# Kernel tuning notes

Hardware: AMD Instinct MI355X
Metric: run time of the kernel (lower is better)

## Reference

```python
import jax, jax.numpy as jnp
import numpy as np

# Standard NF4 quantization codebook (bitsandbytes values)
_NF4_CB = np.array([
    -1.0, -0.6961928009986877, -0.5250730514526367, -0.39491748809814453,
    -0.28444138169288635, -0.18477343022823334, -0.09105003625154495, 0.0,
    0.07958029955625534, 0.16093020141124725, 0.24611230194568634, 0.33791524171829224,
    0.44070982933044434, 0.5626170039176941, 0.7229568362236023, 1.0], dtype=np.float32)

B, L, H, E, DFF = 2, 2048, 2048, 8, 8192
BLK = 512  # NF4 quantization block size (b_idx = h // 512 in kernel)


def setup_inputs() -> dict:
    key = jax.random.key(0)
    ks = jax.random.split(key, 8)
    N = B * L
    x = jax.random.normal(ks[0], (B, L, H), dtype=jnp.float32)
    router_w = jax.random.normal(ks[1], (H, E), dtype=jnp.float32) * 0.02
    # packed NF4: one byte = two 4-bit codebook indices (low nibble -> even h)
    nf4 = jax.random.randint(ks[2], (N, E, H // 2), 0, 256, dtype=jnp.int32)
    mean = jax.random.normal(ks[3], (N, E, H // BLK), dtype=jnp.float32) * 0.01
    std = jax.random.uniform(ks[4], (N, E, H // BLK), dtype=jnp.float32) + 0.5
    codebook = jnp.asarray(_NF4_CB)
    w1 = jax.random.normal(ks[5], (H, DFF), dtype=jnp.float32) * 0.02
    w2 = jax.random.normal(ks[6], (DFF, H), dtype=jnp.float32) * 0.02
    return {"x": x, "router_w": router_w, "nf4": nf4, "mean": mean,
            "std": std, "codebook": codebook, "w1": w1, "w2": w2}


def reference(x, router_w, nf4, mean, std, codebook, w1, w2):
    b, l, h = x.shape
    n = b * l
    e = router_w.shape[1]
    xf = x.reshape(n, h)

    # shared expert MLP (base_mlp): Linear -> GELU -> Linear
    mlp = jax.nn.gelu(xf @ w1) @ w2  # [N, H]

    # router: logits in fp32, softmax, cast to fp16 as the kernel does
    logits = xf @ router_w  # [N, E]
    probs = jax.nn.softmax(logits, axis=-1).astype(jnp.float16).astype(jnp.float32)

    # NF4 unpack: low nibble -> even h, high nibble -> odd h
    low = nf4 & 15
    high = (nf4 >> 4) & 15
    idx = jnp.stack([low, high], axis=-1).reshape(n, e, h)  # interleave -> [N,E,H]
    vals = codebook[idx]  # codebook gather, [N,E,H]

    # per-block (512) rescale: val*std + mean
    nb = mean.shape[-1]
    blk = h // nb
    dq = (vals.reshape(n, e, nb, blk) * std[..., None] + mean[..., None]).reshape(n, e, h)

    # weighted expert mix + MLP residual add
    moe = jnp.einsum('ne,neh->nh', probs, dq)
    return (moe + mlp).reshape(b, l, h)
```

## Files before the change

### kernel.cpp

```cpp
#include <hip/hip_runtime.h>
#include <hip/hip_bf16.h>
#include <hip/hip_fp16.h>

#define H 2048
#define E 8
#define DFF 8192
#define NTOK 4096
#define NB 4

typedef _Float16 f16x8 __attribute__((ext_vector_type(8)));
typedef float f32x4 __attribute__((ext_vector_type(4)));

#define AS1 __attribute__((address_space(1)))
#define AS3 __attribute__((address_space(3)))

__device__ __forceinline__ void gl_lds16(const void* g, void* l) {
    __builtin_amdgcn_global_load_lds((const AS1 unsigned int*)g,
                                     (AS3 unsigned int*)l, 16, 0, 0);
}

__device__ __forceinline__ float gelu_f(float x) {
    float u = 0.7978845608028654f * x * (1.0f + 0.044715f * x * x);
    float t = fabsf(u);
    float e = __expf(-2.0f * t);
    float th = (1.0f - e) / (1.0f + e);
    th = copysignf(th, u);
    return 0.5f * x * (1.0f + th);
}

__global__ __launch_bounds__(256) void router_cast_kernel(
    const float* __restrict__ x, const float* __restrict__ rw,
    float* __restrict__ probs, _Float16* __restrict__ xh)
{
    int n = blockIdx.x, t = threadIdx.x;
    float acc[E];
#pragma unroll
    for (int e = 0; e < E; ++e) acc[e] = 0.f;
    const float* xr = x + (size_t)n * H;
#pragma unroll
    for (int k = 0; k < H / 256; ++k) {
        int h = t + k * 256;
        float xv = xr[h];
        xh[(size_t)n * H + h] = (_Float16)xv;
        const float4* r4 = reinterpret_cast<const float4*>(rw + (size_t)h * E);
        float4 a = r4[0], b = r4[1];
        acc[0] += xv * a.x; acc[1] += xv * a.y; acc[2] += xv * a.z; acc[3] += xv * a.w;
        acc[4] += xv * b.x; acc[5] += xv * b.y; acc[6] += xv * b.z; acc[7] += xv * b.w;
    }
#pragma unroll
    for (int e = 0; e < E; ++e) {
        float v = acc[e];
#pragma unroll
        for (int o = 32; o > 0; o >>= 1) v += __shfl_down(v, o, 64);
        acc[e] = v;
    }
    __shared__ float red[4][E];
    int wave = t >> 6, lane = t & 63;
    if (lane == 0) {
#pragma unroll
        for (int e = 0; e < E; ++e) red[wave][e] = acc[e];
    }
    __syncthreads();
    if (t == 0) {
        float lg[E];
        float mx = -1e30f;
#pragma unroll
        for (int e = 0; e < E; ++e) {
            lg[e] = red[0][e] + red[1][e] + red[2][e] + red[3][e];
            mx = fmaxf(mx, lg[e]);
        }
        float s = 0.f;
#pragma unroll
        for (int e = 0; e < E; ++e) { lg[e] = expf(lg[e] - mx); s += lg[e]; }
        float inv = 1.f / s;
#pragma unroll
        for (int e = 0; e < E; ++e) {
            float p = lg[e] * inv;
            p = __half2float(__float2half(p));
            probs[(size_t)n * E + e] = p;
        }
    }
}

__global__ __launch_bounds__(256) void transpose_cast_kernel(
    const float* __restrict__ src, _Float16* __restrict__ dst, int R, int C)
{
    __shared__ float tile[32][33];
    int tx = threadIdx.x & 31, ty = threadIdx.x >> 5;
    int c0 = blockIdx.x * 32, r0 = blockIdx.y * 32;
#pragma unroll
    for (int i = ty; i < 32; i += 8)
        tile[i][tx] = src[(size_t)(r0 + i) * C + c0 + tx];
    __syncthreads();
#pragma unroll
    for (int i = ty; i < 32; i += 8)
        dst[(size_t)(c0 + i) * R + r0 + tx] = (_Float16)tile[tx][i];
}

__global__ __launch_bounds__(256) void moe_kernel(
    const int* __restrict__ nf4, const float* __restrict__ mean,
    const float* __restrict__ stdv, const float* __restrict__ cb,
    const float* __restrict__ probs, float* __restrict__ moe)
{
    int n = blockIdx.x, t = threadIdx.x;
    __shared__ float cbl[32];
    __shared__ float ps[E][NB];
    __shared__ float cmean[NB];
    if (t < 16) { float v = cb[t]; cbl[t] = v; cbl[t + 16] = v; }
    else if (t >= 32 && t < 64) {
        int e = (t - 32) >> 2, b = t & 3;
        ps[e][b] = probs[(size_t)n * E + e] * stdv[((size_t)n * E + e) * NB + b];
    } else if (t >= 64 && t < 68) {
        int b = t - 64; float s = 0.f;
        for (int e = 0; e < E; ++e)
            s += probs[(size_t)n * E + e] * mean[((size_t)n * E + e) * NB + b];
        cmean[b] = s;
    }
    __syncthreads();
    int cboff = (t & 1) << 4;
    const int* w = nf4 + (size_t)n * (E * H / 2);
    float2* outp = reinterpret_cast<float2*>(moe + (size_t)n * H);
#pragma unroll
    for (int k = 0; k < 4; ++k) {
        int j = t + k * 256;
        float psr[E];
#pragma unroll
        for (int e = 0; e < E; ++e) psr[e] = ps[e][k];
        float cm = cmean[k];
        float aL = cm, aH = cm;
#pragma unroll
        for (int e = 0; e < E; ++e) {
            int word = w[e * (H / 2) + j];
            aL += psr[e] * cbl[(word & 15) + cboff];
            aH += psr[e] * cbl[((word >> 4) & 15) + cboff];
        }
        outp[j] = make_float2(aL, aH);
    }
}

template <int EPI, int MAP>
__global__ __launch_bounds__(512, 2) void gemm8p_kernel(
    const _Float16* __restrict__ A, const _Float16* __restrict__ Bt,
    const float* __restrict__ addsrc, void* __restrict__ outv,
    float* __restrict__ aux, int K, int LDK, int N)
{
    __shared__ uint4 lds_u4[131072 / 16];
    char* lds = (char*)lds_u4;
    char* R0 = lds;
    char* R1 = lds + 65536;

    int t = threadIdx.x;
    int id = blockIdx.x;
    int xcd = id & 7, chunk = id >> 3;
    int by, bx, ks = 0;
    if constexpr (MAP == 0) {
        by = (xcd & 1) * 8 + (chunk & 7);
        bx = (xcd >> 1) * 8 + (chunk >> 3);
    } else {
        by = (xcd >> 1) * 4 + (chunk & 3);
        bx = (xcd & 1) * 4 + ((chunk >> 2) & 3);
        ks = chunk >> 4;
    }
    int m0 = by * 256, n0 = bx * 256;
    int koff = ks * K;

    const unsigned short* sA = (const unsigned short*)A
        + (size_t)(m0 + (t & 255)) * LDK + koff + (t >> 8) * 8;
    const unsigned short* sB = (const unsigned short*)Bt
        + (size_t)(n0 + (t & 255)) * LDK + koff + (t >> 8) * 8;
    unsigned dstT = (unsigned)t * 16;

    int lane = t & 63, wave = t >> 6;
    int wr = wave >> 2, wc = wave & 3;
    int mb = wr * 128, nb = wc * 64;
    int q = lane >> 4, m16 = lane & 15;

    unsigned aBase = (unsigned)(mb + m16) * 16u;
    unsigned bBase = 32768u + (unsigned)(nb + m16) * 16u;

    f32x4 acc[8][4] = {};
    f16x8 af[8], bL[4], bH[4];

#define STG_A(Wb, T, s) do { \
    gl_lds16(sA + (size_t)(T) * 64 + (s) * 16,      (Wb) + (s) * 8192 + dstT); \
    gl_lds16(sA + (size_t)(T) * 64 + (s) * 16 + 16, (Wb) + (s) * 8192 + 8192 + dstT); } while (0)
#define STG_B(Wb, T, s) do { \
    gl_lds16(sB + (size_t)(T) * 64 + (s) * 16,      (Wb) + 32768 + (s) * 8192 + dstT); \
    gl_lds16(sB + (size_t)(T) * 64 + (s) * 16 + 16, (Wb) + 32768 + (s) * 8192 + 8192 + dstT); } while (0)
#define RD_A(Rb, ih) do { \
    _Pragma("unroll") for (int il = 0; il < 4; ++il) \
    _Pragma("unroll") for (int kh = 0; kh < 2; ++kh) \
        af[il * 2 + kh] = *(const f16x8*)((Rb) + aBase + \
            (unsigned)(kh * 16384 + q * 4096 + (ih) * 1024 + il * 256)); } while (0)
#define RD_B(Rb, jh, dst) do { \
    _Pragma("unroll") for (int jl = 0; jl < 2; ++jl) \
    _Pragma("unroll") for (int kh = 0; kh < 2; ++kh) \
        dst[jl * 2 + kh] = *(const f16x8*)((Rb) + bBase + \
            (unsigned)(kh * 16384 + q * 4096 + (jh) * 512 + jl * 256)); } while (0)
#define MMQ(ih, bfr, j0) do { \
    __builtin_amdgcn_s_setprio(1); \
    _Pragma("unroll") for (int il = 0; il < 4; ++il) \
    _Pragma("unroll") for (int jl = 0; jl < 2; ++jl) \
    _Pragma("unroll") for (int kh = 0; kh < 2; ++kh) \
        acc[(ih) * 4 + il][(j0) + jl] = __builtin_amdgcn_mfma_f32_16x16x32_f16( \
            af[il * 2 + kh], bfr[jl * 2 + kh], acc[(ih) * 4 + il][(j0) + jl], 0, 0, 0); \
    __builtin_amdgcn_s_setprio(0); } while (0)
#define BARR  asm volatile("s_barrier" ::: "memory")
#define LGKM0 asm volatile("s_waitcnt lgkmcnt(0)" ::: "memory")

    STG_A(R0, 0, 0); STG_A(R0, 0, 2);
    STG_B(R0, 0, 0); STG_B(R0, 0, 2);
    STG_A(R1, 1, 0);
    asm volatile("s_waitcnt vmcnt(2)" ::: "memory");
    BARR;

    int NIT = K / 128;
    for (int i = 0; i < NIT; ++i) {
        int T0 = 2 * i, T1 = 2 * i + 1;
        bool more = (i + 1 < NIT);

        STG_A(R1, T1, 2);
        RD_A(R0, 0); RD_B(R0, 0, bL);
        BARR; LGKM0;
        MMQ(0, bL, 0);
        BARR;
        STG_B(R1, T1, 0);
        RD_B(R0, 1, bH);
        BARR; LGKM0;
        MMQ(0, bH, 2);
        BARR;
        STG_B(R1, T1, 2);
        RD_A(R0, 1);
        BARR; LGKM0;
        MMQ(1, bH, 2);
        BARR;
        if (more) STG_A(R0, T0 + 2, 0);
        MMQ(1, bL, 0);
        if (more) asm volatile("s_waitcnt vmcnt(2)" ::: "memory");
        else      asm volatile("s_waitcnt vmcnt(0)" ::: "memory");
        BARR;

        if (more) STG_A(R0, T0 + 2, 2);
        RD_A(R1, 0); RD_B(R1, 0, bL);
        BARR; LGKM0;
        MMQ(0, bL, 0);
        BARR;
        if (more) STG_B(R0, T0 + 2, 0);
        RD_B(R1, 1, bH);
        BARR; LGKM0;
        MMQ(0, bH, 2);
        BARR;
        if (more) STG_B(R0, T0 + 2, 2);
        RD_A(R1, 1);
        BARR; LGKM0;
        MMQ(1, bH, 2);
        BARR;
        if (more) STG_A(R1, T1 + 2, 0);
        MMQ(1, bL, 0);
        if (more) asm volatile("s_waitcnt vmcnt(2)" ::: "memory");
        else      asm volatile("s_waitcnt vmcnt(0)" ::: "memory");
        BARR;
    }

#pragma unroll
    for (int i = 0; i < 8; ++i)
#pragma unroll
        for (int j = 0; j < 4; ++j) {
            int row = m0 + mb + i * 16 + q * 4;
            int col = n0 + nb + j * 16 + m16;
#pragma unroll
            for (int rix = 0; rix < 4; ++rix) {
                float v = acc[i][j][rix];
                size_t o = (size_t)(row + rix) * N + col;
                if constexpr (EPI == 0) {
                    ((_Float16*)outv)[o] = (_Float16)gelu_f(v);
                } else {
                    if (ks == 0) ((float*)outv)[o] = v + addsrc[o];
                    else         aux[o] = v;
                }
            }
        }
#undef STG_A
#undef STG_B
#undef RD_A
#undef RD_B
#undef MMQ
#undef BARR
#undef LGKM0
}

__global__ __launch_bounds__(256) void combine_kernel(
    float* __restrict__ out, const float* __restrict__ part)
{
    size_t base = (size_t)blockIdx.x * 256 + threadIdx.x;
    const float4* p4 = (const float4*)part;
    float4* o4 = (float4*)out;
#pragma unroll
    for (int s = 0; s < 4; ++s) {
        size_t i = base + (size_t)s * 524288;
        float4 a = o4[i], b = p4[i];
        o4[i] = make_float4(a.x + b.x, a.y + b.y, a.z + b.z, a.w + b.w);
    }
}

extern "C" void kernel_launch(void* const* d_in, const int* in_sizes, int n_in,
                              void* d_out, int out_size, void* d_ws, size_t ws_size,
                              hipStream_t stream) {
    const float* x    = (const float*)d_in[0];
    const float* rw   = (const float*)d_in[1];
    const int*   nf4  = (const int*)d_in[2];
    const float* mean = (const float*)d_in[3];
    const float* stdv = (const float*)d_in[4];
    const float* cb   = (const float*)d_in[5];
    const float* w1   = (const float*)d_in[6];
    const float* w2   = (const float*)d_in[7];
    float* out = (float*)d_out;

    char* ws = (char*)d_ws;
    float* probs      = (float*)ws;
    float* moe        = (float*)(ws + 131072);
    _Float16* xh      = (_Float16*)(ws + 33685504);
    _Float16* w1t     = (_Float16*)(ws + 50462720);
    _Float16* w2t     = (_Float16*)(ws + 84017152);
    _Float16* hid     = (_Float16*)(ws + 117571584);
    float* pbuf       = (float*)(ws + 50462720);

    router_cast_kernel<<<NTOK, 256, 0, stream>>>(x, rw, probs, xh);
    transpose_cast_kernel<<<dim3(DFF / 32, H / 32), 256, 0, stream>>>(w1, w1t, H, DFF);
    transpose_cast_kernel<<<dim3(H / 32, DFF / 32), 256, 0, stream>>>(w2, w2t, DFF, H);
    moe_kernel<<<NTOK, 256, 0, stream>>>(nf4, mean, stdv, cb, probs, moe);
    gemm8p_kernel<0, 0><<<512, 512, 0, stream>>>(xh, w1t, nullptr, (void*)hid,
                                                 nullptr, H, H, DFF);
    gemm8p_kernel<1, 1><<<256, 512, 0, stream>>>(hid, w2t, moe, (void*)out,
                                                 pbuf, DFF / 2, DFF, H);
    combine_kernel<<<2048, 256, 0, stream>>>(out, pbuf);
}
```

Measured before the change: 790.6 us.

## Fuse router and NF4 MoE kernels, vectorize moe loads and widen transpose tiles

Merges the router/softmax kernel with the NF4 dequant-mix kernel so probabilities stay in shared memory instead of going through a global buffer, saving one launch. The MoE part now reads int4 vectors and writes two float4s per thread rather than strided scalar ints. The weight transpose-cast moves from 32x32 to 64x64 tiles with float4 loads and packed half2 stores. The fused kernel adds an extra barrier and does the NF4 work on the same block as the router reduction.

New measurement: 737.0 us. 6.8% less time.

```diff
diff --git a/kernel.cpp b/kernel.cpp
--- a/kernel.cpp
+++ b/kernel.cpp
@@ -9,6 +9,7 @@
 #define NB 4
 
 typedef _Float16 f16x8 __attribute__((ext_vector_type(8)));
+typedef _Float16 f16x2 __attribute__((ext_vector_type(2)));
 typedef float f32x4 __attribute__((ext_vector_type(4)));
 
 #define AS1 __attribute__((address_space(1)))
@@ -28,11 +29,19 @@
     return 0.5f * x * (1.0f + th);
 }
 
-__global__ __launch_bounds__(256) void router_cast_kernel(
+__global__ __launch_bounds__(256) void router_moe_kernel(
     const float* __restrict__ x, const float* __restrict__ rw,
-    float* __restrict__ probs, _Float16* __restrict__ xh)
+    const int* __restrict__ nf4, const float* __restrict__ mean,
+    const float* __restrict__ stdv, const float* __restrict__ cb,
+    _Float16* __restrict__ xh, float* __restrict__ moe)
 {
     int n = blockIdx.x, t = threadIdx.x;
+    __shared__ float red[4][E];
+    __shared__ float pr[E];
+    __shared__ float cbl[32];
+    __shared__ float ps[E][NB];
+    __shared__ float cmean[NB];
+
     float acc[E];
 #pragma unroll
     for (int e = 0; e < E; ++e) acc[e] = 0.f;
@@ -54,7 +63,6 @@
         for (int o = 32; o > 0; o >>= 1) v += __shfl_down(v, o, 64);
         acc[e] = v;
     }
-    __shared__ float red[4][E];
     int wave = t >> 6, lane = t & 63;
     if (lane == 0) {
 #pragma unroll
@@ -76,65 +84,72 @@
 #pragma unroll
         for (int e = 0; e < E; ++e) {
             float p = lg[e] * inv;
-            p = __half2float(__float2half(p));
-            probs[(size_t)n * E + e] = p;
+            pr[e] = __half2float(__float2half(p));
         }
     }
+    __syncthreads();
+
+    if (t < 16) { float v = cb[t]; cbl[t] = v; cbl[t + 16] = v; }
+    else if (t >= 32 && t < 64) {
+        int e = (t - 32) >> 2, b = t & 3;
+        ps[e][b] = pr[e] * stdv[((size_t)n * E + e) * NB + b];
+    } else if (t >= 64 && t < 68) {
+        int b = t - 64; float s = 0.f;
+        for (int e = 0; e < E; ++e)
+            s += pr[e] * mean[((size_t)n * E + e) * NB + b];
+        cmean[b] = s;
+    }
+    __syncthreads();
+
+    int b = t >> 6;
+    int cboff = (t & 1) << 4;
+    const int4* w4 = reinterpret_cast<const int4*>(nf4 + (size_t)n * (E * H / 2));
+    float o[8];
+    float cm = cmean[b];
+#pragma unroll
+    for (int u = 0; u < 8; ++u) o[u] = cm;
+#pragma unroll
+    for (int e = 0; e < E; ++e) {
+        int4 wv = w4[e * 256 + t];
+        float pse = ps[e][b];
+        int w0 = wv.x, w1 = wv.y, w2 = wv.z, w3 = wv.w;
+        o[0] += pse * cbl[(w0 & 15) + cboff];
+        o[1] += pse * cbl[((w0 >> 4) & 15) + cboff];
+        o[2] += pse * cbl[(w1 & 15) + cboff];
+        o[3] += pse * cbl[((w1 >> 4) & 15) + cboff];
+        o[4] += pse * cbl[(w2 & 15) + cboff];
+        o[5] += pse * cbl[((w2 >> 4) & 15) + cboff];
+        o[6] += pse * cbl[(w3 & 15) + cboff];
+        o[7] += pse * cbl[((w3 >> 4) & 15) + cboff];
+    }
+    float4* op = reinterpret_cast<float4*>(moe + (size_t)n * H + 8 * t);
+    op[0] = make_float4(o[0], o[1], o[2], o[3]);
+    op[1] = make_float4(o[4], o[5], o[6], o[7]);
 }
 
 __global__ __launch_bounds__(256) void transpose_cast_kernel(
     const float* __restrict__ src, _Float16* __restrict__ dst, int R, int C)
 {
-    __shared__ float tile[32][33];
-    int tx = threadIdx.x & 31, ty = threadIdx.x >> 5;
-    int c0 = blockIdx.x * 32, r0 = blockIdx.y * 32;
-#pragma unroll
-    for (int i = ty; i < 32; i += 8)
-        tile[i][tx] = src[(size_t)(r0 + i) * C + c0 + tx];
+    __shared__ float tile[64][65];
+    int t = threadIdx.x;
+    int c0 = blockIdx.x * 64, r0 = blockIdx.y * 64;
+    int ct = (t & 15) * 4, rt = t >> 4;
+#pragma unroll
+    for (int i = 0; i < 4; ++i) {
+        int r = rt + i * 16;
+        float4 v = *reinterpret_cast<const float4*>(src + (size_t)(r0 + r) * C + c0 + ct);
+        tile[r][ct] = v.x; tile[r][ct + 1] = v.y;
+        tile[r][ct + 2] = v.z; tile[r][ct + 3] = v.w;
+    }
     __syncthreads();
-#pragma unroll
-    for (int i = ty; i < 32; i += 8)
-        dst[(size_t)(c0 + i) * R + r0 + tx] = (_Float16)tile[tx][i];
-}
-
-__global__ __launch_bounds__(256) void moe_kernel(
-    const int* __restrict__ nf4, const float* __restrict__ mean,
-    const float* __restrict__ stdv, const float* __restrict__ cb,
-    const float* __restrict__ probs, float* __restrict__ moe)
-{
-    int n = blockIdx.x, t = threadIdx.x;
-    __shared__ float cbl[32];
-    __shared__ float ps[E][NB];
-    __shared__ float cmean[NB];
-    if (t < 16) { float v = cb[t]; cbl[t] = v; cbl[t + 16] = v; }
-    else if (t >= 32 && t < 64) {
-        int e = (t - 32) >> 2, b = t & 3;
-        ps[e][b] = probs[(size_t)n * E + e] * stdv[((size_t)n * E + e) * NB + b];
-    } else if (t >= 64 && t < 68) {
-        int b = t - 64; float s = 0.f;
-        for (int e = 0; e < E; ++e)
-            s += probs[(size_t)n * E + e] * mean[((size_t)n * E + e) * NB + b];
-        cmean[b] = s;
-    }
-    __syncthreads();
-    int cboff = (t & 1) << 4;
-    const int* w = nf4 + (size_t)n * (E * H / 2);
-    float2* outp = reinterpret_cast<float2*>(moe + (size_t)n * H);
-#pragma unroll
-    for (int k = 0; k < 4; ++k) {
-        int j = t + k * 256;
-        float psr[E];
-#pragma unroll
-        for (int e = 0; e < E; ++e) psr[e] = ps[e][k];
-        float cm = cmean[k];
-        float aL = cm, aH = cm;
-#pragma unroll
-        for (int e = 0; e < E; ++e) {
-            int word = w[e * (H / 2) + j];
-            aL += psr[e] * cbl[(word & 15) + cboff];
-            aH += psr[e] * cbl[((word >> 4) & 15) + cboff];
-        }
-        outp[j] = make_float2(aL, aH);
+    int u = (t & 31) * 2, cq = t >> 5;
+#pragma unroll
+    for (int i = 0; i < 8; ++i) {
+        int c = cq + i * 8;
+        f16x2 pk;
+        pk[0] = (_Float16)tile[u][c];
+        pk[1] = (_Float16)tile[u + 1][c];
+        *reinterpret_cast<f16x2*>(dst + (size_t)(c0 + c) * R + r0 + u) = pk;
     }
 }
 
@@ -317,7 +332,6 @@
     float* out = (float*)d_out;
 
     char* ws = (char*)d_ws;
-    float* probs      = (float*)ws;
     float* moe        = (float*)(ws + 131072);
     _Float16* xh      = (_Float16*)(ws + 33685504);
     _Float16* w1t     = (_Float16*)(ws + 50462720);
@@ -325,10 +339,9 @@
     _Float16* hid     = (_Float16*)(ws + 117571584);
     float* pbuf       = (float*)(ws + 50462720);
 
-    router_cast_kernel<<<NTOK, 256, 0, stream>>>(x, rw, probs, xh);
-    transpose_cast_kernel<<<dim3(DFF / 32, H / 32), 256, 0, stream>>>(w1, w1t, H, DFF);
-    transpose_cast_kernel<<<dim3(H / 32, DFF / 32), 256, 0, stream>>>(w2, w2t, DFF, H);
-    moe_kernel<<<NTOK, 256, 0, stream>>>(nf4, mean, stdv, cb, probs, moe);
+    router_moe_kernel<<<NTOK, 256, 0, stream>>>(x, rw, nf4, mean, stdv, cb, xh, moe);
+    transpose_cast_kernel<<<dim3(DFF / 64, H / 64), 256, 0, stream>>>(w1, w1t, H, DFF);
+    transpose_cast_kernel<<<dim3(H / 64, DFF / 64), 256, 0, stream>>>(w2, w2t, DFF, H);
     gemm8p_kernel<0, 0><<<512, 512, 0, stream>>>(xh, w1t, nullptr, (void*)hid,
                                                  nullptr, H, H, DFF);
     gemm8p_kernel<1, 1><<<256, 512, 0, stream>>>(hid, w2t, moe, (void*)out,
```
